# Kernel optimization log

Hardware: AMD Instinct MI355X
Metric: run time of the kernel (lower is better)

## Reference

```python
import jax, jax.numpy as jnp
import numpy as np

B, IN_SIZE, OUT_DIM, RANK = 131072, 128, 128, 4


def setup_inputs() -> dict:
    key = jax.random.key(0)
    ks = jax.random.split(key, 6)
    x = jax.random.normal(ks[0], (B, 3, IN_SIZE), dtype=jnp.float32)
    audio_factor = jax.random.normal(ks[1], (RANK, IN_SIZE + 1, OUT_DIM), dtype=jnp.float32) * 0.1
    video_factor = jax.random.normal(ks[2], (RANK, IN_SIZE + 1, OUT_DIM), dtype=jnp.float32) * 0.1
    text_factor = jax.random.normal(ks[3], (RANK, IN_SIZE + 1, OUT_DIM), dtype=jnp.float32) * 0.1
    fusion_weights = jax.random.normal(ks[4], (1, RANK), dtype=jnp.float32)
    fusion_bias = jax.random.normal(ks[5], (1, OUT_DIM), dtype=jnp.float32)
    return {"x": x, "audio_factor": audio_factor, "video_factor": video_factor,
            "text_factor": text_factor, "fusion_weights": fusion_weights,
            "fusion_bias": fusion_bias}


def reference(x, audio_factor, video_factor, text_factor, fusion_weights, fusion_bias):
    b = x.shape[0]
    ones = jnp.ones((b, 1), dtype=x.dtype)
    # append bias-1 column to each modality: [B, in_size+1]
    ah = jnp.concatenate([ones, x[:, 0, :]], axis=1)
    vh = jnp.concatenate([ones, x[:, 1, :]], axis=1)
    th = jnp.concatenate([ones, x[:, 2, :]], axis=1)
    # batched low-rank projections: [rank, B, out]
    fa = jnp.einsum('bi,rio->rbo', ah, audio_factor)
    fv = jnp.einsum('bi,rio->rbo', vh, video_factor)
    ft = jnp.einsum('bi,rio->rbo', th, text_factor)
    zy = fa * fv * ft  # [rank, B, out]
    # contract rank with fusion weights, add bias: [B, out]
    out = jnp.einsum('r,rbo->bo', fusion_weights[0], zy) + fusion_bias
    y2 = out.reshape(-1, fusion_bias.shape[-1])
    return (y2, y2)
```

## Files before the change

### kernel.cpp

```cpp
#include <hip/hip_runtime.h>


typedef _Float16 half8 __attribute__((ext_vector_type(8)));
typedef float f32x4 __attribute__((ext_vector_type(4)));

#define NB 131072L
#define OUT_OFF (NB * 128L)

static __device__ inline f32x4 splat4(float s) { return (f32x4){s, s, s, s}; }

__global__ void pack_b_kernel(const float* __restrict__ af, const float* __restrict__ vf,
                              const float* __restrict__ tf, _Float16* __restrict__ bpk) {
  int t = blockIdx.x * 256 + threadIdx.x;
  int l = t & 63;
  int ks = (t >> 6) & 3;
  int ot = (t >> 8) & 7;
  int r = (t >> 11) & 3;
  int m = t >> 13;
  const float* f = (m == 0) ? af : ((m == 1) ? vf : tf);
  int i0 = 1 + ks * 32 + (l >> 4) * 8;
  int o = ot * 16 + (l & 15);
  half8 v;
#pragma unroll
  for (int j = 0; j < 8; ++j) v[j] = (_Float16)f[(r * 129 + i0 + j) * 128 + o];
  *(half8*)(bpk + (size_t)t * 8) = v;
}

__global__ __launch_bounds__(256, 3) void lmf_main(
    const float* __restrict__ x, const float* __restrict__ af, const float* __restrict__ vf,
    const float* __restrict__ tf, const float* __restrict__ fw, const float* __restrict__ fb,
    const _Float16* __restrict__ bpk, float* __restrict__ out) {
  __shared__ _Float16 bl[48 * 512];

  const int lane = threadIdx.x & 63;
  const int wv = threadIdx.x >> 6;
  const int W = blockIdx.x * 4 + wv;
  const long row0 = (long)W * 32;
  const int m16 = lane & 15;
  const int q = lane >> 4;

  half8 a[2][3][4];
#pragma unroll
  for (int mt = 0; mt < 2; ++mt) {
    const float* xs = x + (row0 + mt * 16 + m16) * 384 + q * 8;
#pragma unroll
    for (int mod = 0; mod < 3; ++mod) {
#pragma unroll
      for (int ks = 0; ks < 4; ++ks) {
        const float* p = xs + mod * 128 + ks * 32;
        f32x4 p0 = __builtin_nontemporal_load((const f32x4*)p);
        f32x4 p1 = __builtin_nontemporal_load((const f32x4*)(p + 4));
#pragma unroll
        for (int j = 0; j < 4; ++j) {
          a[mt][mod][ks][j] = (_Float16)p0[j];
          a[mt][mod][ks][4 + j] = (_Float16)p1[j];
        }
      }
    }
  }

  const float wr0 = fw[0], wr1 = fw[1], wr2 = fw[2], wr3 = fw[3];
  const float wr[4] = {wr0, wr1, wr2, wr3};

  float* po0 = out + (row0 + q * 4) * 128 + m16;
  float* po1 = out + (row0 + 16 + q * 4) * 128 + m16;
  float* qo0 = po0 + OUT_OFF;
  float* qo1 = po1 + OUT_OFF;

  for (int ot = 0; ot < 8; ++ot) {
#pragma unroll
    for (int i = 0; i < 12; ++i) {
      const _Float16* gp = bpk + (size_t)(((i * 8 + ot) * 2048) + wv * 512 + lane * 8);
      _Float16* lp = bl + (i * 2048 + wv * 512 + lane * 8);
      __builtin_amdgcn_global_load_lds((const __attribute__((address_space(1))) void*)gp,
                                       (__attribute__((address_space(3))) void*)lp, 16, 0, 0);
    }
    __syncthreads();

    const int ocol = ot * 16 + m16;
    f32x4 oacc[2];
    oacc[0] = splat4(fb[ocol]);
    oacc[1] = oacc[0];
#pragma unroll
    for (int r = 0; r < 4; ++r) {
      f32x4 acc[3][2];
      acc[0][0] = splat4(af[r * 16512 + ocol]);
      acc[1][0] = splat4(vf[r * 16512 + ocol]);
      acc[2][0] = splat4(tf[r * 16512 + ocol]);
      acc[0][1] = acc[0][0];
      acc[1][1] = acc[1][0];
      acc[2][1] = acc[2][0];
#pragma unroll
      for (int mod = 0; mod < 3; ++mod) {
        const _Float16* bb = bl + ((mod * 4 + r) * 4) * 512 + lane * 8;
#pragma unroll
        for (int ks = 0; ks < 4; ++ks) {
          half8 bf = *(const half8*)(bb + ks * 512);
          acc[mod][0] =
              __builtin_amdgcn_mfma_f32_16x16x32_f16(a[0][mod][ks], bf, acc[mod][0], 0, 0, 0);
          acc[mod][1] =
              __builtin_amdgcn_mfma_f32_16x16x32_f16(a[1][mod][ks], bf, acc[mod][1], 0, 0, 0);
        }
      }
#pragma unroll
      for (int mt = 0; mt < 2; ++mt) {
#pragma unroll
        for (int g = 0; g < 4; ++g) {
          float pa = acc[0][mt][g];
          float pv = acc[1][mt][g];
          float pt = acc[2][mt][g];
          oacc[mt][g] += wr[r] * (pa * pv * pt);
        }
      }
    }
#pragma unroll
    for (int g = 0; g < 4; ++g) {
      __builtin_nontemporal_store(oacc[0][g], po0 + ot * 16 + g * 128);
      __builtin_nontemporal_store(oacc[1][g], po1 + ot * 16 + g * 128);
      __builtin_nontemporal_store(oacc[0][g], qo0 + ot * 16 + g * 128);
      __builtin_nontemporal_store(oacc[1][g], qo1 + ot * 16 + g * 128);
    }
    __syncthreads();
  }
}

__global__ void lmf_fallback(const float* __restrict__ x, const float* __restrict__ af,
                             const float* __restrict__ vf, const float* __restrict__ tf,
                             const float* __restrict__ fw, const float* __restrict__ fb,
                             float* __restrict__ out) {
  long b = blockIdx.x;
  int o = threadIdx.x;
  __shared__ float xr[384];
  for (int i = threadIdx.x; i < 384; i += 128) xr[i] = x[b * 384 + i];
  __syncthreads();
  float acc = fb[o];
  for (int r = 0; r < 4; ++r) {
    const float* A = af + (long)r * 16512 + o;
    const float* V = vf + (long)r * 16512 + o;
    const float* T = tf + (long)r * 16512 + o;
    float sa = A[0], sv = V[0], st = T[0];
    for (int i = 0; i < 128; ++i) {
      sa += xr[i] * A[(i + 1) * 128];
      sv += xr[128 + i] * V[(i + 1) * 128];
      st += xr[256 + i] * T[(i + 1) * 128];
    }
    acc += fw[r] * sa * sv * st;
  }
  out[b * 128 + o] = acc;
  out[OUT_OFF + b * 128 + o] = acc;
}

extern "C" void kernel_launch(void* const* d_in, const int* in_sizes, int n_in, void* d_out,
                              int out_size, void* d_ws, size_t ws_size, hipStream_t stream) {
  const float* x = (const float*)d_in[0];
  const float* af = (const float*)d_in[1];
  const float* vf = (const float*)d_in[2];
  const float* tf = (const float*)d_in[3];
  const float* fw = (const float*)d_in[4];
  const float* fb = (const float*)d_in[5];
  float* out = (float*)d_out;

  const size_t need = 24576 * 8 * sizeof(_Float16);
  if (ws_size >= need) {
    pack_b_kernel<<<96, 256, 0, stream>>>(af, vf, tf, (_Float16*)d_ws);
    lmf_main<<<1024, 256, 0, stream>>>(x, af, vf, tf, fw, fb, (const _Float16*)d_ws, out);
  } else {
    lmf_fallback<<<dim3(131072), 128, 0, stream>>>(x, af, vf, tf, fw, fb, out);
  }
}
```

Measured before the change: 376.4 us.

## Double-buffer packed factor tiles in LDS and overlap loads with MFMA compute

Splits each output tile's LDS factor buffer into two rank halves, so the next tile's loads can be issued while the current half is computed. Raw barriers and explicit vmcnt waits replace __syncthreads. Bias rows and fusion bias are staged once into LDS instead of being read from global memory each iteration. Occupancy is fixed at 2 waves per EU and setprio is raised around the MFMA bursts. The risks are the hand-tuned waitcnt counts, which depend on the ordering of global_load_lds and stores, and the lower occupancy.

```diff
diff --git a/kernel.cpp b/kernel.cpp
--- a/kernel.cpp
+++ b/kernel.cpp
@@ -8,6 +8,7 @@
 #define OUT_OFF (NB * 128L)
 
 static __device__ inline f32x4 splat4(float s) { return (f32x4){s, s, s, s}; }
+#define CFENCE() asm volatile("" ::: "memory")
 
 __global__ void pack_b_kernel(const float* __restrict__ af, const float* __restrict__ vf,
                               const float* __restrict__ tf, _Float16* __restrict__ bpk) {
@@ -26,11 +27,55 @@
   *(half8*)(bpk + (size_t)t * 8) = v;
 }
 
-__global__ __launch_bounds__(256, 3) void lmf_main(
+#define ISSUE(ot_, h_)                                                                     \
+  do {                                                                                     \
+    _Pragma("unroll") for (int il = 0; il < 6; ++il) {                                     \
+      const int i_ = (il >> 1) * 4 + 2 * (h_) + (il & 1);                                  \
+      const _Float16* gp = bpk + (size_t)(((i_ * 8 + (ot_)) * 2048) + wv * 512 + lane * 8);\
+      _Float16* lp = bl + ((h_)*12288 + il * 2048 + wv * 512 + lane * 8);                  \
+      __builtin_amdgcn_global_load_lds((const __attribute__((address_space(1))) void*)gp,  \
+                                       (__attribute__((address_space(3))) void*)lp, 16, 0, \
+                                       0);                                                 \
+    }                                                                                      \
+  } while (0)
+
+#define COMPUTE_HALF(h_)                                                                   \
+  do {                                                                                     \
+    _Pragma("unroll") for (int rr = 0; rr < 2; ++rr) {                                     \
+      const int r_ = 2 * (h_) + rr;                                                        \
+      f32x4 acc[3][2];                                                                     \
+      _Pragma("unroll") for (int mod = 0; mod < 3; ++mod) {                                \
+        acc[mod][0] = splat4(bias_l[mod * 512 + r_ * 128 + ocol]);                         \
+        acc[mod][1] = acc[mod][0];                                                         \
+      }                                                                                    \
+      __builtin_amdgcn_s_setprio(1);                                                       \
+      _Pragma("unroll") for (int mod = 0; mod < 3; ++mod) {                                \
+        const _Float16* bb = bl + (h_)*12288 + (mod * 2 + rr) * 2048 + lane * 8;           \
+        _Pragma("unroll") for (int ks = 0; ks < 4; ++ks) {                                 \
+          half8 bf = *(const half8*)(bb + ks * 512);      \
+          acc[mod][0] =                                                                    \
+              __builtin_amdgcn_mfma_f32_16x16x32_f16(a[0][mod][ks], bf, acc[mod][0], 0, 0, \
+                                                     0);                                   \
+          acc[mod][1] =                                                                    \
+              __builtin_amdgcn_mfma_f32_16x16x32_f16(a[1][mod][ks], bf, acc[mod][1], 0, 0, \
+                                                     0);                                   \
+        }                                                                                  \
+      }                                                                                    \
+      __builtin_amdgcn_s_setprio(0);                                                       \
+      _Pragma("unroll") for (int mt = 0; mt < 2; ++mt) {                                   \
+        _Pragma("unroll") for (int g = 0; g < 4; ++g) {                                    \
+          oacc[mt][g] += wr[r_] * (acc[0][mt][g] * acc[1][mt][g] * acc[2][mt][g]);         \
+        }                                                                                  \
+      }                                                                                    \
+    }                                                                                      \
+  } while (0)
+
+__global__ __launch_bounds__(256) __attribute__((amdgpu_waves_per_eu(2, 2))) void lmf_main(
     const float* __restrict__ x, const float* __restrict__ af, const float* __restrict__ vf,
     const float* __restrict__ tf, const float* __restrict__ fw, const float* __restrict__ fb,
     const _Float16* __restrict__ bpk, float* __restrict__ out) {
-  __shared__ _Float16 bl[48 * 512];
+  __shared__ _Float16 bl[2 * 12288];
+  __shared__ float bias_l[1664];
 
   const int lane = threadIdx.x & 63;
   const int wv = threadIdx.x >> 6;
@@ -39,6 +84,19 @@
   const int m16 = lane & 15;
   const int q = lane >> 4;
 
+  for (int idx = threadIdx.x; idx < 1664; idx += 256) {
+    float v;
+    if (idx < 1536) {
+      const int mod = idx >> 9, rem = idx & 511;
+      const float* f = (mod == 0) ? af : ((mod == 1) ? vf : tf);
+      v = f[(rem >> 7) * 16512 + (rem & 127)];
+    } else {
+      v = fb[idx - 1536];
+    }
+    bias_l[idx] = v;
+  }
+  __syncthreads();
+
   half8 a[2][3][4];
 #pragma unroll
   for (int mt = 0; mt < 2; ++mt) {
@@ -58,61 +116,52 @@
       }
     }
   }
-
-  const float wr0 = fw[0], wr1 = fw[1], wr2 = fw[2], wr3 = fw[3];
-  const float wr[4] = {wr0, wr1, wr2, wr3};
+#pragma unroll
+  for (int mt = 0; mt < 2; ++mt)
+#pragma unroll
+    for (int mod = 0; mod < 3; ++mod)
+#pragma unroll
+      for (int ks = 0; ks < 4; ++ks) asm volatile("" : "+v"(a[mt][mod][ks]));
+
+  const float wr[4] = {fw[0], fw[1], fw[2], fw[3]};
 
   float* po0 = out + (row0 + q * 4) * 128 + m16;
   float* po1 = out + (row0 + 16 + q * 4) * 128 + m16;
   float* qo0 = po0 + OUT_OFF;
   float* qo1 = po1 + OUT_OFF;
 
+  CFENCE();
+  ISSUE(0, 0);
+  ISSUE(0, 1);
+
+#pragma unroll 1
   for (int ot = 0; ot < 8; ++ot) {
-#pragma unroll
-    for (int i = 0; i < 12; ++i) {
-      const _Float16* gp = bpk + (size_t)(((i * 8 + ot) * 2048) + wv * 512 + lane * 8);
-      _Float16* lp = bl + (i * 2048 + wv * 512 + lane * 8);
-      __builtin_amdgcn_global_load_lds((const __attribute__((address_space(1))) void*)gp,
-                                       (__attribute__((address_space(3))) void*)lp, 16, 0, 0);
-    }
-    __syncthreads();
-
     const int ocol = ot * 16 + m16;
+
+    if (ot == 0) {
+      asm volatile("s_waitcnt vmcnt(6)" ::: "memory");
+    } else {
+      asm volatile("s_waitcnt vmcnt(12)" ::: "memory");
+    }
+    __builtin_amdgcn_s_barrier();
+    CFENCE();
     f32x4 oacc[2];
-    oacc[0] = splat4(fb[ocol]);
+    oacc[0] = splat4(bias_l[1536 + ocol]);
     oacc[1] = oacc[0];
-#pragma unroll
-    for (int r = 0; r < 4; ++r) {
-      f32x4 acc[3][2];
-      acc[0][0] = splat4(af[r * 16512 + ocol]);
-      acc[1][0] = splat4(vf[r * 16512 + ocol]);
-      acc[2][0] = splat4(tf[r * 16512 + ocol]);
-      acc[0][1] = acc[0][0];
-      acc[1][1] = acc[1][0];
-      acc[2][1] = acc[2][0];
-#pragma unroll
-      for (int mod = 0; mod < 3; ++mod) {
-        const _Float16* bb = bl + ((mod * 4 + r) * 4) * 512 + lane * 8;
-#pragma unroll
-        for (int ks = 0; ks < 4; ++ks) {
-          half8 bf = *(const half8*)(bb + ks * 512);
-          acc[mod][0] =
-              __builtin_amdgcn_mfma_f32_16x16x32_f16(a[0][mod][ks], bf, acc[mod][0], 0, 0, 0);
-          acc[mod][1] =
-              __builtin_amdgcn_mfma_f32_16x16x32_f16(a[1][mod][ks], bf, acc[mod][1], 0, 0, 0);
-        }
-      }
-#pragma unroll
-      for (int mt = 0; mt < 2; ++mt) {
-#pragma unroll
-        for (int g = 0; g < 4; ++g) {
-          float pa = acc[0][mt][g];
-          float pv = acc[1][mt][g];
-          float pt = acc[2][mt][g];
-          oacc[mt][g] += wr[r] * (pa * pv * pt);
-        }
-      }
-    }
+    COMPUTE_HALF(0);
+    CFENCE();
+    __builtin_amdgcn_s_barrier();
+    CFENCE();
+    if (ot < 7) ISSUE(ot + 1, 0);
+
+    if (ot < 7) {
+      asm volatile("s_waitcnt vmcnt(6)" ::: "memory");
+    } else {
+      asm volatile("s_waitcnt vmcnt(0)" ::: "memory");
+    }
+    __builtin_amdgcn_s_barrier();
+    CFENCE();
+    COMPUTE_HALF(1);
 #pragma unroll
     for (int g = 0; g < 4; ++g) {
       __builtin_nontemporal_store(oacc[0][g], po0 + ot * 16 + g * 128);
@@ -120,7 +169,10 @@
       __builtin_nontemporal_store(oacc[0][g], qo0 + ot * 16 + g * 128);
       __builtin_nontemporal_store(oacc[1][g], qo1 + ot * 16 + g * 128);
     }
-    __syncthreads();
+    CFENCE();
+    __builtin_amdgcn_s_barrier();
+    CFENCE();
+    if (ot < 7) ISSUE(ot + 1, 1);
   }
 }
 
```

After: 359.4 us. -4.5%, faster.

## Load packed B fragments directly from global into registers, dropping LDS staging

Applied to the files above, without the earlier changes.

Removes the shared-memory staging of packed fp16 factor fragments and the two block barriers per output tile. Each wave now loads its B fragments straight from global memory (L1/L2-resident, about 384 KB) into registers, batched before the MFMA chain, and the ot loop is fully unrolled. Occupancy is set to 2 waves per EU to give room for the larger register footprint. In exchange, every wave issues redundant global loads of the same B data, where before the four waves shared one LDS copy, and occupancy may drop.

```diff
diff --git a/kernel.cpp b/kernel.cpp
--- a/kernel.cpp
+++ b/kernel.cpp
@@ -26,16 +26,14 @@
   *(half8*)(bpk + (size_t)t * 8) = v;
 }
 
-__global__ __launch_bounds__(256, 3) void lmf_main(
+__global__ __launch_bounds__(256) __attribute__((amdgpu_waves_per_eu(2, 2))) void lmf_main(
     const float* __restrict__ x, const float* __restrict__ af, const float* __restrict__ vf,
     const float* __restrict__ tf, const float* __restrict__ fw, const float* __restrict__ fb,
     const _Float16* __restrict__ bpk, float* __restrict__ out) {
-  __shared__ _Float16 bl[48 * 512];
-
   const int lane = threadIdx.x & 63;
   const int wv = threadIdx.x >> 6;
-  const int W = blockIdx.x * 4 + wv;
-  const long row0 = (long)W * 32;
+  const long W = (long)blockIdx.x * 4 + wv;
+  const long row0 = W * 32;
   const int m16 = lane & 15;
   const int q = lane >> 4;
 
@@ -59,24 +57,17 @@
     }
   }
 
-  const float wr0 = fw[0], wr1 = fw[1], wr2 = fw[2], wr3 = fw[3];
-  const float wr[4] = {wr0, wr1, wr2, wr3};
+  const float wr[4] = {fw[0], fw[1], fw[2], fw[3]};
 
   float* po0 = out + (row0 + q * 4) * 128 + m16;
   float* po1 = out + (row0 + 16 + q * 4) * 128 + m16;
   float* qo0 = po0 + OUT_OFF;
   float* qo1 = po1 + OUT_OFF;
 
+  const _Float16* bp = bpk + lane * 8;
+
+#pragma unroll
   for (int ot = 0; ot < 8; ++ot) {
-#pragma unroll
-    for (int i = 0; i < 12; ++i) {
-      const _Float16* gp = bpk + (size_t)(((i * 8 + ot) * 2048) + wv * 512 + lane * 8);
-      _Float16* lp = bl + (i * 2048 + wv * 512 + lane * 8);
-      __builtin_amdgcn_global_load_lds((const __attribute__((address_space(1))) void*)gp,
-                                       (__attribute__((address_space(3))) void*)lp, 16, 0, 0);
-    }
-    __syncthreads();
-
     const int ocol = ot * 16 + m16;
     f32x4 oacc[2];
     oacc[0] = splat4(fb[ocol]);
@@ -90,26 +81,28 @@
       acc[0][1] = acc[0][0];
       acc[1][1] = acc[1][0];
       acc[2][1] = acc[2][0];
+      half8 bf[3][4];
 #pragma unroll
       for (int mod = 0; mod < 3; ++mod) {
-        const _Float16* bb = bl + ((mod * 4 + r) * 4) * 512 + lane * 8;
+        const _Float16* bb = bp + (size_t)((((mod * 4 + r) * 8 + ot) * 4) * 512);
+#pragma unroll
+        for (int ks = 0; ks < 4; ++ks) bf[mod][ks] = *(const half8*)(bb + ks * 512);
+      }
+#pragma unroll
+      for (int mod = 0; mod < 3; ++mod) {
 #pragma unroll
         for (int ks = 0; ks < 4; ++ks) {
-          half8 bf = *(const half8*)(bb + ks * 512);
-          acc[mod][0] =
-              __builtin_amdgcn_mfma_f32_16x16x32_f16(a[0][mod][ks], bf, acc[mod][0], 0, 0, 0);
-          acc[mod][1] =
-              __builtin_amdgcn_mfma_f32_16x16x32_f16(a[1][mod][ks], bf, acc[mod][1], 0, 0, 0);
+          acc[mod][0] = __builtin_amdgcn_mfma_f32_16x16x32_f16(a[0][mod][ks], bf[mod][ks],
+                                                               acc[mod][0], 0, 0, 0);
+          acc[mod][1] = __builtin_amdgcn_mfma_f32_16x16x32_f16(a[1][mod][ks], bf[mod][ks],
+                                                               acc[mod][1], 0, 0, 0);
         }
       }
 #pragma unroll
       for (int mt = 0; mt < 2; ++mt) {
 #pragma unroll
         for (int g = 0; g < 4; ++g) {
-          float pa = acc[0][mt][g];
-          float pv = acc[1][mt][g];
-          float pt = acc[2][mt][g];
-          oacc[mt][g] += wr[r] * (pa * pv * pt);
+          oacc[mt][g] += wr[r] * (acc[0][mt][g] * acc[1][mt][g] * acc[2][mt][g]);
         }
       }
     }
@@ -120,7 +113,6 @@
       __builtin_nontemporal_store(oacc[0][g], qo0 + ot * 16 + g * 128);
       __builtin_nontemporal_store(oacc[1][g], qo1 + ot * 16 + g * 128);
     }
-    __syncthreads();
   }
 }
 
```

After: 375.3 us. About the same (-0.3%).
